# Kernel optimization log

Measured on AMD Instinct MI355X. Metric: run time of the kernel, lower is better.

Reference implementation:

```python
import jax, jax.numpy as jnp
import numpy as np

B, T, N, F, UNITS = 64, 12, 512, 64, 64

def setup_inputs() -> dict:
    key = jax.random.key(0)
    ks = jax.random.split(key, 9)
    inputs = jax.random.normal(ks[0], (B, T, N, F), dtype=jnp.float32)
    # binary k-hop adjacency mask with self loops (K.to_dense(calculate_adjacency_k(...)))
    A = (jax.random.uniform(ks[1], (N, N)) < 0.05).astype(jnp.float32)
    A = jnp.maximum(A, jnp.eye(N, dtype=jnp.float32))
    W1 = jax.random.normal(ks[2], (T, 1), dtype=jnp.float32) * 0.3
    W2 = jax.random.normal(ks[3], (F, T), dtype=jnp.float32) * 0.1
    W3 = jax.random.normal(ks[4], (F, 1), dtype=jnp.float32) * 0.1
    Ve = jax.random.normal(ks[5], (N, N), dtype=jnp.float32) * 0.05
    be = jax.random.normal(ks[6], (N, N), dtype=jnp.float32) * 0.05
    kernel = jax.random.normal(ks[7], (F, UNITS), dtype=jnp.float32) * 0.1
    bias = jax.random.normal(ks[8], (UNITS,), dtype=jnp.float32) * 0.1
    return {"inputs": inputs, "A": A, "W1": W1, "W2": W2, "W3": W3,
            "Ve": Ve, "be": be, "kernel": kernel, "bias": bias}

def reference(inputs, A, W1, W2, W3, Ve, be, kernel, bias):
    # inputs: (B, T, N, F)
    # lhs: permute->(B,N,F,T), dot W1, squeeze, dot W2 -> (B, N, T)
    r1 = jnp.einsum('btnf,t->bnf', inputs, W1[:, 0])
    lhs = jnp.einsum('bnf,ft->bnt', r1, W2)
    # rhs: dot W3, squeeze -> (B, T, N)
    rhs = jnp.einsum('btnf,f->btn', inputs, W3[:, 0])
    # batch_dot -> (B, N, N)
    product = jnp.einsum('bnt,btm->bnm', lhs, rhs)
    E = jnp.einsum('jk,bkm->bjm', Ve, jax.nn.sigmoid(product + be))
    masked = E + (-1e16) * (1.0 - A)            # adjacency mask
    attn = jax.nn.softmax(masked, axis=-1)       # (B, N, N)
    # graph conv: (B,N,N) x (B,T,N,F) -> (B,T,N,F)
    conv = jnp.einsum('bjk,btkf->btjf', attn, inputs)
    out = jnp.einsum('btjf,fu->btju', conv, kernel) + bias
    return out  # activation=None -> linear
```

## Files before the change

kernel.cpp:

```cpp
#include <hip/hip_runtime.h>
#include <hip/hip_bf16.h>
#include <cstdint>

constexpr int BB = 64;
constexpr int TT = 12;
constexpr int NN = 512;
constexpr int FF = 64;
constexpr int UU = 64;
constexpr int MAXNZ = 128;

constexpr size_t OF_LHS   = 0;
constexpr size_t OF_RHS   = 393216;
constexpr size_t OF_BET   = 786432;
constexpr size_t OF_EVALS = 1048576;
constexpr size_t OB_NNZ   = 20971520;
constexpr size_t OB_CIDX  = 20973568;
constexpr size_t OB_CCNT  = 21235712;
constexpr size_t OB_COLJ  = 21237760;
constexpr size_t OB_XT    = 21516288;
constexpr size_t XT_BYTES = (size_t)BB * NN * TT * FF * 2;
constexpr size_t OB_KF    = 71847936;
constexpr size_t KF_BYTES = 8 * 64 * 8 * 2;

typedef __attribute__((ext_vector_type(8))) short bf16x8;
typedef __attribute__((ext_vector_type(4))) float f32x4;

__device__ __forceinline__ float wred_sum(float v) {
  #pragma unroll
  for (int off = 32; off; off >>= 1) v += __shfl_xor(v, off, 64);
  return v;
}

__device__ __forceinline__ float bflo(unsigned u) {
  return __uint_as_float(u << 16);
}
__device__ __forceinline__ float bfhi(unsigned u) {
  return __uint_as_float(u & 0xFFFF0000u);
}

__global__ __launch_bounds__(256) void k_lhs_rhs(
    const float* __restrict__ x, const float* __restrict__ W1,
    const float* __restrict__ W2, const float* __restrict__ W3,
    float* __restrict__ lhs, float* __restrict__ rhsS,
    unsigned short* __restrict__ xT)
{
  int unit = blockIdx.x * 4 + (threadIdx.x >> 6);
  int lane = threadIdx.x & 63;
  int b = unit >> 9, n = unit & 511;

  const float* xb = x + ((size_t)b * TT * NN + n) * FF + lane;
  float xv[12];
  #pragma unroll
  for (int t = 0; t < 12; ++t) xv[t] = xb[(size_t)t * NN * FF];

  if (xT) {
    unsigned short* xo = xT + (size_t)unit * (TT * FF) + lane;
    #pragma unroll
    for (int t = 0; t < 12; ++t) {
      __hip_bfloat16 h = __float2bfloat16(xv[t]);
      xo[t * FF] = *reinterpret_cast<unsigned short*>(&h);
    }
  }

  float r1 = 0.f;
  #pragma unroll
  for (int t = 0; t < 12; ++t) r1 += xv[t] * W1[t];

  float w3 = W3[lane];

  float myl = 0.f, myr = 0.f;
  #pragma unroll
  for (int t = 0; t < 12; ++t) {
    float a = r1 * W2[lane * 12 + t];
    float c = xv[t] * w3;
    a = wred_sum(a);
    c = wred_sum(c);
    if (lane == t) { myl = a; myr = c; }
  }
  if (lane < 12) {
    lhs[(size_t)unit * 12 + lane]  = myl;
    rhsS[(size_t)unit * 12 + lane] = myr;
  }
}

__global__ __launch_bounds__(256) void k_transpose(
    const float* __restrict__ be, float* __restrict__ beT,
    const float* __restrict__ K, unsigned short* __restrict__ KF)
{
  if (blockIdx.x == NN * NN / 256) {
    if (KF) {
      for (int idx = threadIdx.x; idx < 512; idx += 256) {
        int frag = idx >> 6, l = idx & 63;
        int kk = frag >> 2, nt = frag & 3;
        int u = nt * 16 + (l & 15);
        unsigned short* dst = KF + (size_t)idx * 8;
        for (int e = 0; e < 8; ++e) {
          int f = kk * 32 + (l >> 4) * 8 + e;
          __hip_bfloat16 h = __float2bfloat16(K[f * 64 + u]);
          dst[e] = *reinterpret_cast<unsigned short*>(&h);
        }
      }
    }
    return;
  }
  int i = blockIdx.x * 256 + threadIdx.x;
  int k = i >> 9, m = i & 511;
  beT[m * 512 + k] = be[i];
}

__global__ void k_build_idx(const float* __restrict__ A,
                            int* __restrict__ nnz, int* __restrict__ cidx)
{
  int j = blockIdx.x;
  int lane = threadIdx.x;
  unsigned long long lt = (1ull << lane) - 1ull;
  int base = 0;
  for (int c = 0; c < 8; ++c) {
    int m = c * 64 + lane;
    bool p = A[(size_t)j * 512 + m] > 0.5f;
    unsigned long long mask = __ballot(p);
    int pos = base + __popcll(mask & lt);
    if (p && pos < MAXNZ) cidx[j * MAXNZ + pos] = m;
    base += __popcll(mask);
  }
  if (lane == 0) nnz[j] = base > MAXNZ ? MAXNZ : base;
}

__global__ void k_build_col(const int* __restrict__ nnz, const int* __restrict__ cidx,
                            int* __restrict__ ccnt, unsigned* __restrict__ colj)
{
  int j = blockIdx.x;
  int lane = threadIdx.x;
  int cnt = nnz[j];
  for (int s = lane; s < cnt; s += 64) {
    int m = cidx[j * MAXNZ + s];
    int pos = atomicAdd(&ccnt[m], 1);
    if (pos < MAXNZ) colj[m * MAXNZ + pos] = (unsigned)j | ((unsigned)s << 16);
  }
}

__global__ __launch_bounds__(256) void k_product_E3(
    const float* __restrict__ lhs, const float* __restrict__ rhsS,
    const float* __restrict__ beT, const float* __restrict__ Ve,
    const int* __restrict__ ccnt, const unsigned* __restrict__ colj,
    float* __restrict__ evals)
{
  int b  = blockIdx.x;
  int mc = blockIdx.y;

  __shared__ __align__(16) float sL[4][512];
  __shared__ float rh[16 * 12];

  int tid = threadIdx.x;
  int wave = tid >> 6, lane = tid & 63;
  int grp = lane >> 4, lg = lane & 15;

  float l0[12], l1[12];
  {
    const float* p0 = lhs + ((size_t)b * 512 + tid) * 12;
    const float* p1 = lhs + ((size_t)b * 512 + tid + 256) * 12;
    #pragma unroll
    for (int t = 0; t < 12; ++t) { l0[t] = p0[t]; l1[t] = p1[t]; }
  }
  if (tid < 192) rh[tid] = rhsS[((size_t)b * 512 + mc * 16) * 12 + tid];
  __syncthreads();

  for (int g = 0; g < 4; ++g) {
    if (g) __syncthreads();
    #pragma unroll
    for (int mm = 0; mm < 4; ++mm) {
      int m = mc * 16 + g * 4 + mm;
      float p0 = beT[m * 512 + tid];
      float p1 = beT[m * 512 + tid + 256];
      const float* rw = &rh[(g * 4 + mm) * 12];
      #pragma unroll
      for (int t = 0; t < 12; ++t) {
        p0 = fmaf(l0[t], rw[t], p0);
        p1 = fmaf(l1[t], rw[t], p1);
      }
      sL[mm][tid]       = 1.0f / (1.0f + __expf(-p0));
      sL[mm][tid + 256] = 1.0f / (1.0f + __expf(-p1));
    }
    __syncthreads();

    int m = mc * 16 + g * 4 + wave;
    int cnt = ccnt[m];
    if (cnt > MAXNZ) cnt = MAXNZ;
    const float4* sw4 = (const float4*)sL[wave];
    for (int e = grp; e < cnt; e += 4) {
      unsigned pk = colj[m * MAXNZ + e];
      int j = pk & 0xffff, slot = (int)(pk >> 16);
      const float4* vr4 = (const float4*)(Ve + (size_t)j * 512);
      float a = 0.f;
      #pragma unroll
      for (int i = 0; i < 8; ++i) {
        float4 v4 = vr4[lg + 16 * i];
        float4 s4 = sw4[lg + 16 * i];
        a = fmaf(v4.x, s4.x, a);
        a = fmaf(v4.y, s4.y, a);
        a = fmaf(v4.z, s4.z, a);
        a = fmaf(v4.w, s4.w, a);
      }
      #pragma unroll
      for (int off = 8; off; off >>= 1) a += __shfl_xor(a, off, 64);
      if (lg == 0) evals[((size_t)b * 512 + j) * MAXNZ + slot] = a;
    }
  }
}

__global__ __launch_bounds__(256) void k_out12(
    const unsigned short* __restrict__ xT,
    const int* __restrict__ nnz, const int* __restrict__ cidx,
    const float* __restrict__ evals,
    const unsigned short* __restrict__ KF, const float* __restrict__ bias,
    float* __restrict__ out)
{
  int tid = threadIdx.x;
  int wv = tid >> 6, lane = tid & 63;
  int bid = blockIdx.x;
  int sbid = (bid & 7) * 1024 + (bid >> 3);
  int unit = sbid * 4 + wv;
  int b = unit >> 9, j = unit & 511;

  __shared__ unsigned short convB[4][16][80];
  __shared__ float valL[4][MAXNZ];
  __shared__ int   idxL[4][MAXNZ];

  int cnt = nnz[j];
  for (int s = lane; s < cnt; s += 64) {
    idxL[wv][s] = cidx[j * MAXNZ + s];
    valL[wv][s] = evals[(size_t)unit * MAXNZ + s];
  }
  {
    float v0 = lane < cnt        ? valL[wv][lane]      : -__builtin_inff();
    float v1 = (lane + 64) < cnt ? valL[wv][lane + 64] : -__builtin_inff();
    float mx = fmaxf(v0, v1);
    #pragma unroll
    for (int off = 32; off; off >>= 1) mx = fmaxf(mx, __shfl_xor(mx, off, 64));
    float e0 = lane < cnt        ? __expf(v0 - mx) : 0.f;
    float e1 = (lane + 64) < cnt ? __expf(v1 - mx) : 0.f;
    float ssum = wred_sum(e0 + e1);
    float inv = 1.0f / ssum;
    if (lane < cnt)        valL[wv][lane]      = e0 * inv;
    if ((lane + 64) < cnt) valL[wv][lane + 64] = e1 * inv;
  }

  float2 acc[6];
  #pragma unroll
  for (int i = 0; i < 6; ++i) acc[i] = make_float2(0.f, 0.f);

  const unsigned* xb = reinterpret_cast<const unsigned*>(
      xT + (size_t)b * NN * (TT * FF));

  int s = 0;
  for (; s + 1 < cnt; s += 2) {
    int   k0 = idxL[wv][s],     k1 = idxL[wv][s + 1];
    float v0 = valL[wv][s],     v1 = valL[wv][s + 1];
    const unsigned* p0 = xb + k0 * 384 + lane;
    const unsigned* p1 = xb + k1 * 384 + lane;
    unsigned a0 = p0[0],   a1 = p0[64],  a2 = p0[128],
             a3 = p0[192], a4 = p0[256], a5 = p0[320];
    unsigned c0 = p1[0],   c1 = p1[64],  c2 = p1[128],
             c3 = p1[192], c4 = p1[256], c5 = p1[320];
    acc[0].x = fmaf(v0, bflo(a0), acc[0].x); acc[0].y = fmaf(v0, bfhi(a0), acc[0].y);
    acc[1].x = fmaf(v0, bflo(a1), acc[1].x); acc[1].y = fmaf(v0, bfhi(a1), acc[1].y);
    acc[2].x = fmaf(v0, bflo(a2), acc[2].x); acc[2].y = fmaf(v0, bfhi(a2), acc[2].y);
    acc[3].x = fmaf(v0, bflo(a3), acc[3].x); acc[3].y = fmaf(v0, bfhi(a3), acc[3].y);
    acc[4].x = fmaf(v0, bflo(a4), acc[4].x); acc[4].y = fmaf(v0, bfhi(a4), acc[4].y);
    acc[5].x = fmaf(v0, bflo(a5), acc[5].x); acc[5].y = fmaf(v0, bfhi(a5), acc[5].y);
    acc[0].x = fmaf(v1, bflo(c0), acc[0].x); acc[0].y = fmaf(v1, bfhi(c0), acc[0].y);
    acc[1].x = fmaf(v1, bflo(c1), acc[1].x); acc[1].y = fmaf(v1, bfhi(c1), acc[1].y);
    acc[2].x = fmaf(v1, bflo(c2), acc[2].x); acc[2].y = fmaf(v1, bfhi(c2), acc[2].y);
    acc[3].x = fmaf(v1, bflo(c3), acc[3].x); acc[3].y = fmaf(v1, bfhi(c3), acc[3].y);
    acc[4].x = fmaf(v1, bflo(c4), acc[4].x); acc[4].y = fmaf(v1, bfhi(c4), acc[4].y);
    acc[5].x = fmaf(v1, bflo(c5), acc[5].x); acc[5].y = fmaf(v1, bfhi(c5), acc[5].y);
  }
  if (s < cnt) {
    int   k0 = idxL[wv][s];
    float v0 = valL[wv][s];
    const unsigned* p0 = xb + k0 * 384 + lane;
    unsigned a0 = p0[0],   a1 = p0[64],  a2 = p0[128],
             a3 = p0[192], a4 = p0[256], a5 = p0[320];
    acc[0].x = fmaf(v0, bflo(a0), acc[0].x); acc[0].y = fmaf(v0, bfhi(a0), acc[0].y);
    acc[1].x = fmaf(v0, bflo(a1), acc[1].x); acc[1].y = fmaf(v0, bfhi(a1), acc[1].y);
    acc[2].x = fmaf(v0, bflo(a2), acc[2].x); acc[2].y = fmaf(v0, bfhi(a2), acc[2].y);
    acc[3].x = fmaf(v0, bflo(a3), acc[3].x); acc[3].y = fmaf(v0, bfhi(a3), acc[3].y);
    acc[4].x = fmaf(v0, bflo(a4), acc[4].x); acc[4].y = fmaf(v0, bfhi(a4), acc[4].y);
    acc[5].x = fmaf(v0, bflo(a5), acc[5].x); acc[5].y = fmaf(v0, bfhi(a5), acc[5].y);
  }

  int half = lane >> 5, fl = lane & 31;
  {
    unsigned short* cb = &convB[wv][0][0];
    #pragma unroll
    for (int i = 0; i < 6; ++i) {
      int t = 2 * i + half;
      __hip_bfloat16 hx = __float2bfloat16(acc[i].x);
      __hip_bfloat16 hy = __float2bfloat16(acc[i].y);
      unsigned pkd = (unsigned)*reinterpret_cast<unsigned short*>(&hx)
                   | ((unsigned)*reinterpret_cast<unsigned short*>(&hy) << 16);
      *reinterpret_cast<unsigned*>(&cb[t * 80 + fl * 2]) = pkd;
    }
  }

  int arow = lane & 15, agrp = lane >> 4;
  bf16x8 afrag0 = *reinterpret_cast<const bf16x8*>(&convB[wv][arow][agrp * 8]);
  bf16x8 afrag1 = *reinterpret_cast<const bf16x8*>(&convB[wv][arow][32 + agrp * 8]);
  const bf16x8* kf = reinterpret_cast<const bf16x8*>(KF);

  #pragma unroll
  for (int nt = 0; nt < 4; ++nt) {
    f32x4 accT = {0.f, 0.f, 0.f, 0.f};
    accT = __builtin_amdgcn_mfma_f32_16x16x32_bf16(afrag0, kf[(0 * 4 + nt) * 64 + lane], accT, 0, 0, 0);
    accT = __builtin_amdgcn_mfma_f32_16x16x32_bf16(afrag1, kf[(1 * 4 + nt) * 64 + lane], accT, 0, 0, 0);
    int u = nt * 16 + arow;
    float bb = bias[u];
    #pragma unroll
    for (int r = 0; r < 4; ++r) {
      int t = agrp * 4 + r;
      if (t < 12)
        out[((size_t)(b * TT + t) * NN + j) * UU + u] = accT[r] + bb;
    }
  }
}

__global__ __launch_bounds__(256) void k_out3f(
    const float* __restrict__ x,
    const int* __restrict__ nnz, const int* __restrict__ cidx,
    const float* __restrict__ evals,
    const float* __restrict__ K, const float* __restrict__ bias,
    float* __restrict__ out)
{
  int wv = threadIdx.x >> 6, lane = threadIdx.x & 63;
  int bid = blockIdx.x;
  int sbid = (bid & 7) * 1024 + (bid >> 3);
  int unit = sbid * 4 + wv;
  int b = unit >> 9, j = unit & 511;

  __shared__ float convL[4][12][64];
  __shared__ float valL[4][MAXNZ];
  __shared__ int   idxL[4][MAXNZ];

  int cnt = nnz[j];
  for (int s = lane; s < cnt; s += 64) {
    idxL[wv][s] = cidx[j * MAXNZ + s];
    valL[wv][s] = evals[(size_t)unit * MAXNZ + s];
  }
  {
    float v0 = lane < cnt        ? valL[wv][lane]      : -__builtin_inff();
    float v1 = (lane + 64) < cnt ? valL[wv][lane + 64] : -__builtin_inff();
    float mx = fmaxf(v0, v1);
    #pragma unroll
    for (int off = 32; off; off >>= 1) mx = fmaxf(mx, __shfl_xor(mx, off, 64));
    float e0 = lane < cnt        ? __expf(v0 - mx) : 0.f;
    float e1 = (lane + 64) < cnt ? __expf(v1 - mx) : 0.f;
    float ssum = wred_sum(e0 + e1);
    float inv = 1.0f / ssum;
    if (lane < cnt)        valL[wv][lane]      = e0 * inv;
    if ((lane + 64) < cnt) valL[wv][lane + 64] = e1 * inv;
  }

  float acc[12];
  #pragma unroll
  for (int t = 0; t < 12; ++t) acc[t] = 0.f;

  const float* xb = x + (size_t)b * TT * NN * FF + lane;
  for (int s = 0; s < cnt; ++s) {
    float v = valL[wv][s];
    const float* xk = xb + (size_t)idxL[wv][s] * FF;
    #pragma unroll
    for (int t = 0; t < 12; ++t)
      acc[t] = fmaf(v, xk[(size_t)t * NN * FF], acc[t]);
  }
  #pragma unroll
  for (int t = 0; t < 12; ++t) convL[wv][t][lane] = acc[t];

  float bs = bias[lane];
  float o[12];
  #pragma unroll
  for (int t = 0; t < 12; ++t) o[t] = bs;
  __syncthreads();

  #pragma unroll
  for (int ft = 0; ft < 4; ++ft) {
    float kc[16];
    #pragma unroll
    for (int i = 0; i < 16; ++i) kc[i] = K[(ft * 16 + i) * 64 + lane];
    #pragma unroll
    for (int t = 0; t < 12; ++t) {
      const float4* cv = (const float4*)&convL[wv][t][ft * 16];
      float4 c0 = cv[0], c1 = cv[1], c2 = cv[2], c3 = cv[3];
      float o_ = o[t];
      o_ = fmaf(c0.x, kc[0],  o_); o_ = fmaf(c0.y, kc[1],  o_);
      o_ = fmaf(c0.z, kc[2],  o_); o_ = fmaf(c0.w, kc[3],  o_);
      o_ = fmaf(c1.x, kc[4],  o_); o_ = fmaf(c1.y, kc[5],  o_);
      o_ = fmaf(c1.z, kc[6],  o_); o_ = fmaf(c1.w, kc[7],  o_);
      o_ = fmaf(c2.x, kc[8],  o_); o_ = fmaf(c2.y, kc[9],  o_);
      o_ = fmaf(c2.z, kc[10], o_); o_ = fmaf(c2.w, kc[11], o_);
      o_ = fmaf(c3.x, kc[12], o_); o_ = fmaf(c3.y, kc[13], o_);
      o_ = fmaf(c3.z, kc[14], o_); o_ = fmaf(c3.w, kc[15], o_);
      o[t] = o_;
    }
  }

  #pragma unroll
  for (int t = 0; t < 12; ++t)
    out[((size_t)(b * TT + t) * NN + j) * UU + lane] = o[t];
}

extern "C" void kernel_launch(void* const* d_in, const int* in_sizes, int n_in,
                              void* d_out, int out_size, void* d_ws, size_t ws_size,
                              hipStream_t stream)
{
  const float* x    = (const float*)d_in[0];
  const float* A    = (const float*)d_in[1];
  const float* W1   = (const float*)d_in[2];
  const float* W2   = (const float*)d_in[3];
  const float* W3   = (const float*)d_in[4];
  const float* Ve   = (const float*)d_in[5];
  const float* be   = (const float*)d_in[6];
  const float* K    = (const float*)d_in[7];
  const float* bias = (const float*)d_in[8];
  float* out = (float*)d_out;

  char* ws = (char*)d_ws;
  float* lhs   = (float*)ws + OF_LHS;
  float* rhsS  = (float*)ws + OF_RHS;
  float* beT   = (float*)ws + OF_BET;
  float* evals = (float*)ws + OF_EVALS;
  int*      nnz  = (int*)(ws + OB_NNZ);
  int*      cidx = (int*)(ws + OB_CIDX);
  int*      ccnt = (int*)(ws + OB_CCNT);
  unsigned* colj = (unsigned*)(ws + OB_COLJ);
  unsigned short* xT = (unsigned short*)(ws + OB_XT);
  unsigned short* KF = (unsigned short*)(ws + OB_KF);

  const bool use_xt = ws_size >= OB_KF + KF_BYTES;

  hipMemsetAsync(ccnt, 0, NN * sizeof(int), stream);

  k_lhs_rhs<<<dim3(BB * NN / 4), dim3(256), 0, stream>>>(
      x, W1, W2, W3, lhs, rhsS, use_xt ? xT : nullptr);
  k_transpose<<<dim3(NN * NN / 256 + 1), dim3(256), 0, stream>>>(
      be, beT, K, use_xt ? KF : nullptr);
  k_build_idx<<<dim3(NN), dim3(64), 0, stream>>>(A, nnz, cidx);
  k_build_col<<<dim3(NN), dim3(64), 0, stream>>>(nnz, cidx, ccnt, colj);
  k_product_E3<<<dim3(BB, NN / 16), dim3(256), 0, stream>>>(lhs, rhsS, beT, Ve, ccnt, colj, evals);
  if (use_xt)
    k_out12<<<dim3(BB * NN / 4), dim3(256), 0, stream>>>(xT, nnz, cidx, evals, KF, bias, out);
  else
    k_out3f<<<dim3(BB * NN / 4), dim3(256), 0, stream>>>(x, nnz, cidx, evals, K, bias, out);
}
```

Baseline: 219.1 us.

## Compute all sixteen sigmoid columns at once and give each column a 16-lane group

The E kernel now computes the sigmoid columns for all 16 m values into a larger shared buffer before a single barrier, replacing four compute/sync phases. Each 16-lane group then owns one m column, instead of four groups sharing a wave-level column. The sparse dot-product loop handles two nonzeros per iteration so more independent Ve loads are in flight. The cost is 32KB of shared memory per block, which can lower occupancy, and group loop lengths vary with per-column nonzero counts, which can cause divergence within a wave.

```diff
diff --git a/kernel.cpp b/kernel.cpp
--- a/kernel.cpp
+++ b/kernel.cpp
@@ -139,7 +139,7 @@
   }
 }
 
-__global__ __launch_bounds__(256) void k_product_E3(
+__global__ __launch_bounds__(256) void k_product_E4(
     const float* __restrict__ lhs, const float* __restrict__ rhsS,
     const float* __restrict__ beT, const float* __restrict__ Ve,
     const int* __restrict__ ccnt, const unsigned* __restrict__ colj,
@@ -148,12 +148,10 @@
   int b  = blockIdx.x;
   int mc = blockIdx.y;
 
-  __shared__ __align__(16) float sL[4][512];
+  __shared__ __align__(16) float sL[16][512];
   __shared__ float rh[16 * 12];
 
   int tid = threadIdx.x;
-  int wave = tid >> 6, lane = tid & 63;
-  int grp = lane >> 4, lg = lane & 15;
 
   float l0[12], l1[12];
   {
@@ -165,46 +163,72 @@
   if (tid < 192) rh[tid] = rhsS[((size_t)b * 512 + mc * 16) * 12 + tid];
   __syncthreads();
 
-  for (int g = 0; g < 4; ++g) {
-    if (g) __syncthreads();
-    #pragma unroll
-    for (int mm = 0; mm < 4; ++mm) {
-      int m = mc * 16 + g * 4 + mm;
-      float p0 = beT[m * 512 + tid];
-      float p1 = beT[m * 512 + tid + 256];
-      const float* rw = &rh[(g * 4 + mm) * 12];
-      #pragma unroll
-      for (int t = 0; t < 12; ++t) {
-        p0 = fmaf(l0[t], rw[t], p0);
-        p1 = fmaf(l1[t], rw[t], p1);
-      }
-      sL[mm][tid]       = 1.0f / (1.0f + __expf(-p0));
-      sL[mm][tid + 256] = 1.0f / (1.0f + __expf(-p1));
-    }
-    __syncthreads();
-
-    int m = mc * 16 + g * 4 + wave;
-    int cnt = ccnt[m];
-    if (cnt > MAXNZ) cnt = MAXNZ;
-    const float4* sw4 = (const float4*)sL[wave];
-    for (int e = grp; e < cnt; e += 4) {
-      unsigned pk = colj[m * MAXNZ + e];
-      int j = pk & 0xffff, slot = (int)(pk >> 16);
-      const float4* vr4 = (const float4*)(Ve + (size_t)j * 512);
-      float a = 0.f;
-      #pragma unroll
-      for (int i = 0; i < 8; ++i) {
-        float4 v4 = vr4[lg + 16 * i];
-        float4 s4 = sw4[lg + 16 * i];
-        a = fmaf(v4.x, s4.x, a);
-        a = fmaf(v4.y, s4.y, a);
-        a = fmaf(v4.z, s4.z, a);
-        a = fmaf(v4.w, s4.w, a);
-      }
-      #pragma unroll
-      for (int off = 8; off; off >>= 1) a += __shfl_xor(a, off, 64);
-      if (lg == 0) evals[((size_t)b * 512 + j) * MAXNZ + slot] = a;
-    }
+  #pragma unroll 4
+  for (int mm = 0; mm < 16; ++mm) {
+    int m = mc * 16 + mm;
+    float p0 = beT[m * 512 + tid];
+    float p1 = beT[m * 512 + tid + 256];
+    const float* rw = &rh[mm * 12];
+    #pragma unroll
+    for (int t = 0; t < 12; ++t) {
+      p0 = fmaf(l0[t], rw[t], p0);
+      p1 = fmaf(l1[t], rw[t], p1);
+    }
+    sL[mm][tid]       = 1.0f / (1.0f + __expf(-p0));
+    sL[mm][tid + 256] = 1.0f / (1.0f + __expf(-p1));
+  }
+  __syncthreads();
+
+  int gi = tid >> 4, lg = tid & 15;
+  int m = mc * 16 + gi;
+  int cnt = ccnt[m];
+  if (cnt > MAXNZ) cnt = MAXNZ;
+  const float4* sw4 = (const float4*)sL[gi];
+
+  int e = 0;
+  for (; e + 1 < cnt; e += 2) {
+    unsigned pk0 = colj[m * MAXNZ + e];
+    unsigned pk1 = colj[m * MAXNZ + e + 1];
+    int j0 = pk0 & 0xffff, s0 = (int)(pk0 >> 16);
+    int j1 = pk1 & 0xffff, s1 = (int)(pk1 >> 16);
+    const float4* va = (const float4*)(Ve + (size_t)j0 * 512);
+    const float4* vb = (const float4*)(Ve + (size_t)j1 * 512);
+    float a = 0.f, c = 0.f;
+    #pragma unroll
+    for (int i = 0; i < 8; ++i) {
+      float4 s4 = sw4[lg + 16 * i];
+      float4 v4 = va[lg + 16 * i];
+      float4 w4 = vb[lg + 16 * i];
+      a = fmaf(v4.x, s4.x, a); a = fmaf(v4.y, s4.y, a);
+      a = fmaf(v4.z, s4.z, a); a = fmaf(v4.w, s4.w, a);
+      c = fmaf(w4.x, s4.x, c); c = fmaf(w4.y, s4.y, c);
+      c = fmaf(w4.z, s4.z, c); c = fmaf(w4.w, s4.w, c);
+    }
+    #pragma unroll
+    for (int off = 8; off; off >>= 1) {
+      a += __shfl_xor(a, off, 64);
+      c += __shfl_xor(c, off, 64);
+    }
+    if (lg == 0) {
+      evals[((size_t)b * 512 + j0) * MAXNZ + s0] = a;
+      evals[((size_t)b * 512 + j1) * MAXNZ + s1] = c;
+    }
+  }
+  if (e < cnt) {
+    unsigned pk0 = colj[m * MAXNZ + e];
+    int j0 = pk0 & 0xffff, s0 = (int)(pk0 >> 16);
+    const float4* va = (const float4*)(Ve + (size_t)j0 * 512);
+    float a = 0.f;
+    #pragma unroll
+    for (int i = 0; i < 8; ++i) {
+      float4 s4 = sw4[lg + 16 * i];
+      float4 v4 = va[lg + 16 * i];
+      a = fmaf(v4.x, s4.x, a); a = fmaf(v4.y, s4.y, a);
+      a = fmaf(v4.z, s4.z, a); a = fmaf(v4.w, s4.w, a);
+    }
+    #pragma unroll
+    for (int off = 8; off; off >>= 1) a += __shfl_xor(a, off, 64);
+    if (lg == 0) evals[((size_t)b * 512 + j0) * MAXNZ + s0] = a;
   }
 }
 
@@ -445,7 +469,7 @@
       be, beT, K, use_xt ? KF : nullptr);
   k_build_idx<<<dim3(NN), dim3(64), 0, stream>>>(A, nnz, cidx);
   k_build_col<<<dim3(NN), dim3(64), 0, stream>>>(nnz, cidx, ccnt, colj);
-  k_product_E3<<<dim3(BB, NN / 16), dim3(256), 0, stream>>>(lhs, rhsS, beT, Ve, ccnt, colj, evals);
+  k_product_E4<<<dim3(BB, NN / 16), dim3(256), 0, stream>>>(lhs, rhsS, beT, Ve, ccnt, colj, evals);
   if (use_xt)
     k_out12<<<dim3(BB * NN / 4), dim3(256), 0, stream>>>(xT, nnz, cidx, evals, KF, bias, out);
   else
```

New measurement: 222.8 us (median of 2 runs). About the same (+1.7%).
